# Optimization experiments

Measured on AMD Instinct MI355X. Metric: run time of the kernel, lower is better.

## Reference

```python
import jax, jax.numpy as jnp
import numpy as np

M, N, IN_DIM, NITER = 32, 32, 1024, 100
ALPHA, SIGMA = 0.3, 16.0  # sigma default = max(m, n) / 2
BATCH = 16384


def setup_inputs() -> dict:
    key = jax.random.key(0)
    k1, k2 = jax.random.split(key)
    x = jax.random.normal(k1, (BATCH, IN_DIM), dtype=jnp.float32)
    weights = jax.random.normal(k2, (IN_DIM, M * N), dtype=jnp.float32)
    ii, jj = jnp.meshgrid(jnp.arange(M), jnp.arange(N), indexing='ij')
    locations = jnp.stack([ii.ravel(), jj.ravel()], axis=1).astype(jnp.int32)  # (m*n, 2), row-major like the generator
    return {"x": x, "weights": weights, "locations": locations, "current_iter": 10}


def reference(x, weights, locations, current_iter):
    # x: (B, in_dim); weights: (in_dim, m*n); locations: (m*n, 2)
    B = x.shape[0]
    # Euclidean distances from each sample to each neuron, via ||a-b||^2 expansion
    x2 = jnp.sum(x * x, axis=1, keepdims=True)            # (B, 1)
    w2 = jnp.sum(weights * weights, axis=0)[None, :]      # (1, m*n)
    d2 = jnp.clip(x2 + w2 - 2.0 * (x @ weights), 0.0, None)
    dists = jnp.sqrt(d2)                                  # (B, m*n)
    loss_per = jnp.min(dists, axis=1)                     # (B,)
    bmu_index = jnp.argmin(dists, axis=1)                 # (B,)
    iter_correction = 1.0 - current_iter / NITER
    lr = ALPHA * iter_correction
    sigma = SIGMA * iter_correction
    loc_f = locations.astype(jnp.float32)                 # (m*n, 2)
    bmu_loc = loc_f[bmu_index]                            # (B, 2)
    # squared grid distance of every neuron to each sample's BMU
    dsq = jnp.sum((loc_f[None, :, :] - bmu_loc[:, None, :]) ** 2, axis=2)  # (B, m*n)
    lr_locations = jnp.exp(-dsq / (sigma * sigma)) * lr   # (B, m*n)
    # delta[i,k] = (1/B) * sum_b lr_locations[b,k] * (x[b,i] - weights[i,k])
    # computed without materializing the (B, in_dim, m*n) broadcast tensor
    pos = jnp.einsum('bk,bi->ik', lr_locations, x)        # (in_dim, m*n)
    neg = weights * jnp.sum(lr_locations, axis=0)[None, :]
    delta = (pos - neg) / B
    new_weights = weights + delta
    loss = jnp.sum(loss_per) / B
    return loss, new_weights
```

## Files before the change

### kernel.cpp

```cpp
#include <hip/hip_runtime.h>

typedef unsigned short u16;
typedef short bf16x8 __attribute__((ext_vector_type(8)));
typedef float f32x4 __attribute__((ext_vector_type(4)));

#define BATCH   16384
#define INDIM   1024
#define KNEUR   1024

__device__ __forceinline__ u16 f2bf(float f) {
  union { float f; unsigned u; } v; v.f = f;
  unsigned r = v.u + 0x7FFFu + ((v.u >> 16) & 1u);
  return (u16)(r >> 16);
}
__device__ __forceinline__ float bf2f(u16 h) {
  union { unsigned u; float f; } v; v.u = ((unsigned)h) << 16; return v.f;
}

#define GLDS(gp, lp) __builtin_amdgcn_global_load_lds( \
  (const __attribute__((address_space(1))) void*)(gp), \
  (__attribute__((address_space(3))) void*)(lp), 16, 0, 0)

__global__ void k_conv_x(const float* __restrict__ x, u16* __restrict__ xb,
                         float* __restrict__ x2) {
  int b = blockIdx.x;
  int t = threadIdx.x;
  const float4 v = *(const float4*)(x + (size_t)b * INDIM + t * 4);
  u16 o0 = f2bf(v.x), o1 = f2bf(v.y), o2 = f2bf(v.z), o3 = f2bf(v.w);
  ushort4 o; o.x = o0; o.y = o1; o.z = o2; o.w = o3;
  *(ushort4*)(xb + (size_t)b * INDIM + t * 4) = o;
  float s = v.x * v.x + v.y * v.y + v.z * v.z + v.w * v.w;
  for (int m = 32; m; m >>= 1) s += __shfl_xor(s, m, 64);
  __shared__ float ws_[4];
  if ((t & 63) == 0) ws_[t >> 6] = s;
  __syncthreads();
  if (t == 0) x2[b] = ws_[0] + ws_[1] + ws_[2] + ws_[3];
}

__global__ void k_trans_w(const float* __restrict__ w, u16* __restrict__ wt) {
  __shared__ float tile[64][65];
  int bi = blockIdx.x & 15;
  int bj = blockIdx.x >> 4;
  int tx = threadIdx.x & 63, ty = threadIdx.x >> 6;
  int i0 = bj * 64, k0 = bi * 64;
  for (int r = ty; r < 64; r += 4)
    tile[r][tx] = w[(size_t)(i0 + r) * KNEUR + k0 + tx];
  __syncthreads();
  for (int r = ty; r < 64; r += 4)
    wt[(size_t)(k0 + r) * INDIM + i0 + tx] = f2bf(tile[tx][r]);
}

__global__ void k_w2(const float* __restrict__ w, float* __restrict__ w2) {
  int tx = threadIdx.x & 63, ty = threadIdx.x >> 6;
  int k = blockIdx.x * 64 + tx;
  float s = 0.f;
  for (int i = ty * 256; i < ty * 256 + 256; ++i) {
    float v = w[(size_t)i * KNEUR + k];
    s += v * v;
  }
  __shared__ float red[4][64];
  red[ty][tx] = s;
  __syncthreads();
  if (ty == 0) w2[k] = red[0][tx] + red[1][tx] + red[2][tx] + red[3][tx];
}

__global__ void k_T(const int* __restrict__ loc, const int* __restrict__ itp,
                    u16* __restrict__ Tb, float* __restrict__ Tf) {
  int id = blockIdx.x * 256 + threadIdx.x;
  int c = id >> 10, k = id & 1023;
  float corr = 1.f - (float)itp[0] / 100.f;
  float lr = 0.3f * corr;
  float sig = 16.f * corr;
  float inv_s2 = 1.f / (sig * sig);
  int di = loc[2 * c] - loc[2 * k];
  int dj = loc[2 * c + 1] - loc[2 * k + 1];
  float v = lr * __expf(-(float)(di * di + dj * dj) * inv_s2);
  Tf[id] = v;
  Tb[id] = f2bf(v);
}

template <int EPI>
__global__ __launch_bounds__(256, 2)
void k_gemm(const u16* __restrict__ A, const u16* __restrict__ Bm,
            const float* __restrict__ x2, const float* __restrict__ w2,
            float* __restrict__ pmin, int* __restrict__ pidx,
            const float* __restrict__ Wf, const float* __restrict__ S,
            float* __restrict__ outw) {
  __shared__ __align__(16) u16 ldsA[128 * 64];
  __shared__ __align__(16) u16 ldsB[128 * 64];
  __shared__ float s_rv[2][128];
  __shared__ int   s_ri[2][128];

  int bid = blockIdx.x;
  int mb, nb;
  if (EPI == 1) {
    int swz = (bid & 7) * 128 + (bid >> 3);
    mb = swz >> 3; nb = swz & 7;
  } else {
    mb = bid >> 3; nb = bid & 7;
  }
  int lane = threadIdx.x & 63;
  int wid = threadIdx.x >> 6;
  int wr = wid >> 1, wc = wid & 1;

  f32x4 acc[4][4];
  #pragma unroll
  for (int i = 0; i < 4; ++i)
    #pragma unroll
    for (int j = 0; j < 4; ++j) { acc[i][j][0] = 0.f; acc[i][j][1] = 0.f; acc[i][j][2] = 0.f; acc[i][j][3] = 0.f; }

  const size_t rowA0 = (size_t)mb * 128;
  const size_t rowB0 = (size_t)nb * 128;

  for (int kt = 0; kt < 16; ++kt) {
    int k0 = kt * 64;
    __syncthreads();
    #pragma unroll
    for (int q = 0; q < 4; ++q) {
      int p = q * 256 + wid * 64 + lane;
      int row = p >> 3;
      int clog = (p & 7) ^ (row & 7);
      GLDS(A + (rowA0 + row) * 1024 + k0 + clog * 8,
           ldsA + (size_t)(q * 256 + wid * 64) * 8);
    }
    #pragma unroll
    for (int q = 0; q < 4; ++q) {
      int p = q * 256 + wid * 64 + lane;
      int row = p >> 3;
      int clog = (p & 7) ^ (row & 7);
      GLDS(Bm + (rowB0 + row) * 1024 + k0 + clog * 8,
           ldsB + (size_t)(q * 256 + wid * 64) * 8);
    }
    __syncthreads();
    #pragma unroll
    for (int kk = 0; kk < 2; ++kk) {
      bf16x8 af[4], bfr[4];
      #pragma unroll
      for (int mt = 0; mt < 4; ++mt) {
        int row = wr * 64 + mt * 16 + (lane & 15);
        int ch = (kk * 4 + (lane >> 4)) ^ (row & 7);
        af[mt] = *(const bf16x8*)(ldsA + row * 64 + ch * 8);
      }
      #pragma unroll
      for (int nt = 0; nt < 4; ++nt) {
        int row = wc * 64 + nt * 16 + (lane & 15);
        int ch = (kk * 4 + (lane >> 4)) ^ (row & 7);
        bfr[nt] = *(const bf16x8*)(ldsB + row * 64 + ch * 8);
      }
      #pragma unroll
      for (int mt = 0; mt < 4; ++mt)
        #pragma unroll
        for (int nt = 0; nt < 4; ++nt)
          acc[mt][nt] = __builtin_amdgcn_mfma_f32_16x16x32_bf16(af[mt], bfr[nt], acc[mt][nt], 0, 0, 0);
    }
  }

  if (EPI == 1) {
    int g = lane >> 4;
    int li = lane & 15;
    #pragma unroll
    for (int mt = 0; mt < 4; ++mt) {
      #pragma unroll
      for (int r = 0; r < 4; ++r) {
        int rowl = wr * 64 + mt * 16 + g * 4 + r;
        float xv = x2[rowA0 + rowl];
        float v = 1e30f; int vi = 0;
        #pragma unroll
        for (int nt = 0; nt < 4; ++nt) {
          int col = (int)rowB0 + wc * 64 + nt * 16 + li;
          float d2 = xv + w2[col] - 2.f * acc[mt][nt][r];
          if (d2 < v) { v = d2; vi = col; }
        }
        #pragma unroll
        for (int m = 1; m < 16; m <<= 1) {
          float ov = __shfl_xor(v, m, 64);
          int oi = __shfl_xor(vi, m, 64);
          if (ov < v || (ov == v && oi < vi)) { v = ov; vi = oi; }
        }
        if (li == 0) { s_rv[wc][rowl] = v; s_ri[wc][rowl] = vi; }
      }
    }
    __syncthreads();
    int t = threadIdx.x;
    if (t < 128) {
      float v0 = s_rv[0][t], v1 = s_rv[1][t];
      int i0 = s_ri[0][t], i1 = s_ri[1][t];
      float v = v0; int vi = i0;
      if (v1 < v0) { v = v1; vi = i1; }
      size_t brow = rowA0 + t;
      pmin[brow * 8 + nb] = v;
      pidx[brow * 8 + nb] = vi;
    }
  } else {
    const float invB = 1.f / (float)BATCH;
    #pragma unroll
    for (int mt = 0; mt < 4; ++mt)
      #pragma unroll
      for (int nt = 0; nt < 4; ++nt)
        #pragma unroll
        for (int r = 0; r < 4; ++r) {
          int i = (int)rowA0 + wr * 64 + mt * 16 + (lane >> 4) * 4 + r;
          int k = (int)rowB0 + wc * 64 + nt * 16 + (lane & 15);
          float wv = Wf[(size_t)i * KNEUR + k];
          float P = acc[mt][nt][r];
          outw[(size_t)i * KNEUR + k] = wv + (P - wv * S[k]) * invB;
        }
  }
}

__global__ void k_bmu(const float* __restrict__ pmin, const int* __restrict__ pidx,
                      int* __restrict__ bmu, float* __restrict__ lpart) {
  int b = blockIdx.x * 256 + threadIdx.x;
  float v = 1e30f; int vi = 0;
  #pragma unroll
  for (int j = 0; j < 8; ++j) {
    float pv = pmin[(size_t)b * 8 + j];
    if (pv < v) { v = pv; vi = pidx[(size_t)b * 8 + j]; }
  }
  bmu[b] = vi;
  float d = sqrtf(fmaxf(v, 0.f));
  __shared__ float red[256];
  red[threadIdx.x] = d;
  __syncthreads();
  for (int s = 128; s > 0; s >>= 1) {
    if (threadIdx.x < s) red[threadIdx.x] += red[threadIdx.x + s];
    __syncthreads();
  }
  if (threadIdx.x == 0) lpart[blockIdx.x] = red[0];
}

__global__ void k_loss(const float* __restrict__ lpart, float* __restrict__ out) {
  if (threadIdx.x == 0) {
    float s = 0.f;
    for (int i = 0; i < 64; ++i) s += lpart[i];
    out[0] = s * (1.f / (float)BATCH);
  }
}

__global__ __launch_bounds__(256)
void k_xsum(const int* __restrict__ bmu, const u16* __restrict__ xb,
            u16* __restrict__ xst, float* __restrict__ cntf) {
  int c = blockIdx.x;
  int t = threadIdx.x;
  __shared__ u16 list[BATCH];
  __shared__ int scan[256];
  __shared__ int s_total;
  int cnt = 0;
  for (int j = 0; j < 64; ++j) cnt += (bmu[j * 256 + t] == c);
  scan[t] = cnt;
  __syncthreads();
  for (int off = 1; off < 256; off <<= 1) {
    int v = scan[t];
    int va = (t >= off) ? scan[t - off] : 0;
    __syncthreads();
    scan[t] = v + va;
    __syncthreads();
  }
  int pos = scan[t] - cnt;
  if (t == 255) s_total = scan[255];
  __syncthreads();
  int total = s_total;
  for (int j = 0; j < 64; ++j) {
    int b = j * 256 + t;
    if (bmu[b] == c) list[pos++] = (u16)b;
  }
  __syncthreads();
  float a0 = 0.f, a1 = 0.f, a2 = 0.f, a3 = 0.f;
  for (int m = 0; m < total; ++m) {
    int b = list[m];
    ushort4 v = *(const ushort4*)(xb + (size_t)b * INDIM + t * 4);
    a0 += bf2f(v.x); a1 += bf2f(v.y); a2 += bf2f(v.z); a3 += bf2f(v.w);
  }
  xst[(size_t)(4 * t + 0) * KNEUR + c] = f2bf(a0);
  xst[(size_t)(4 * t + 1) * KNEUR + c] = f2bf(a1);
  xst[(size_t)(4 * t + 2) * KNEUR + c] = f2bf(a2);
  xst[(size_t)(4 * t + 3) * KNEUR + c] = f2bf(a3);
  if (t == 0) cntf[c] = (float)total;
}

__global__ void k_spart(const float* __restrict__ cntf, const float* __restrict__ Tf,
                        float* __restrict__ spart) {
  int cchunk = blockIdx.x >> 2;
  int kb = blockIdx.x & 3;
  int k = kb * 256 + threadIdx.x;
  float s = 0.f;
  for (int c = cchunk * 64; c < cchunk * 64 + 64; ++c)
    s += cntf[c] * Tf[(size_t)c * KNEUR + k];
  spart[cchunk * KNEUR + k] = s;
}
__global__ void k_sfinal(const float* __restrict__ spart, float* __restrict__ S) {
  int k = blockIdx.x * 256 + threadIdx.x;
  float s = 0.f;
  #pragma unroll
  for (int j = 0; j < 16; ++j) s += spart[j * KNEUR + k];
  S[k] = s;
}

extern "C" void kernel_launch(void* const* d_in, const int* in_sizes, int n_in,
                              void* d_out, int out_size, void* d_ws, size_t ws_size,
                              hipStream_t stream) {
  const float* x = (const float*)d_in[0];
  const float* w = (const float*)d_in[1];
  const int* loc = (const int*)d_in[2];
  const int* it = (const int*)d_in[3];
  float* out = (float*)d_out;

  char* ws = (char*)d_ws;
  size_t off = 0;
  auto alloc = [&](size_t bytes) -> void* {
    void* p = ws + off;
    off += (bytes + 255) & ~(size_t)255;
    return p;
  };
  u16* xb    = (u16*)  alloc((size_t)BATCH * INDIM * 2);
  u16* wt    = (u16*)  alloc((size_t)KNEUR * INDIM * 2);
  u16* Tb    = (u16*)  alloc((size_t)KNEUR * KNEUR * 2);
  float* Tf  = (float*)alloc((size_t)KNEUR * KNEUR * 4);
  u16* xst   = (u16*)  alloc((size_t)INDIM * KNEUR * 2);
  float* x2  = (float*)alloc((size_t)BATCH * 4);
  float* w2  = (float*)alloc((size_t)KNEUR * 4);
  float* pmin= (float*)alloc((size_t)BATCH * 8 * 4);
  int* pidx  = (int*)  alloc((size_t)BATCH * 8 * 4);
  int* bmu   = (int*)  alloc((size_t)BATCH * 4);
  float* cntf= (float*)alloc((size_t)KNEUR * 4);
  float* spart=(float*)alloc((size_t)16 * KNEUR * 4);
  float* S   = (float*)alloc((size_t)KNEUR * 4);
  float* lpart=(float*)alloc(64 * 4);
  if (off > ws_size) return;

  k_conv_x<<<BATCH, 256, 0, stream>>>(x, xb, x2);
  k_trans_w<<<256, 256, 0, stream>>>(w, wt);
  k_w2<<<16, 256, 0, stream>>>(w, w2);
  k_T<<<4096, 256, 0, stream>>>(loc, it, Tb, Tf);
  k_gemm<1><<<1024, 256, 0, stream>>>(xb, wt, x2, w2, pmin, pidx, nullptr, nullptr, nullptr);
  k_bmu<<<64, 256, 0, stream>>>(pmin, pidx, bmu, lpart);
  k_loss<<<1, 64, 0, stream>>>(lpart, out);
  k_xsum<<<1024, 256, 0, stream>>>(bmu, xb, xst, cntf);
  k_spart<<<64, 256, 0, stream>>>(cntf, Tf, spart);
  k_sfinal<<<4, 256, 0, stream>>>(spart, S);
  k_gemm<0><<<64, 256, 0, stream>>>(xst, Tb, nullptr, nullptr, nullptr, nullptr, w, S, out + 1);
}
```

Baseline: 165.2 us.

## Replace per-neuron BMU scan with counting-sort permutation and atomic segmented sums

The per-BMU x-sum is restructured. Before, each of 1024 blocks scanned all 16384 BMU indices to build its own member list. Now a global histogram, a prefix scan and an atomic placement build a permutation sorted by BMU. Blocks then sum contiguous 16-sample chunks and flush partial sums to an fp32 buffer with atomics, and a tiled transpose produces the bf16 xst layout. This removes the redundant full scan done in every block and the load imbalance across neurons, at the cost of extra launches, a 4MB zeroing pass, fp32 atomics and a non-deterministic summation order.

```diff
diff --git a/kernel.cpp b/kernel.cpp
--- a/kernel.cpp
+++ b/kernel.cpp
@@ -237,45 +237,82 @@
   }
 }
 
+__global__ void k_zero(float* __restrict__ p, int n) {
+  int i = blockIdx.x * 256 + threadIdx.x;
+  if (i < n) p[i] = 0.f;
+}
+
+__global__ void k_count(const int* __restrict__ bmu, int* __restrict__ cnt) {
+  int b = blockIdx.x * 256 + threadIdx.x;
+  atomicAdd(&cnt[bmu[b]], 1);
+}
+
+__global__ void k_offsets(const int* __restrict__ cnt, int* __restrict__ cursor,
+                          float* __restrict__ cntf) {
+  __shared__ int s[1024];
+  int t = threadIdx.x;
+  int v = cnt[t];
+  cntf[t] = (float)v;
+  s[t] = v;
+  __syncthreads();
+  for (int off = 1; off < 1024; off <<= 1) {
+    int a = s[t];
+    int b = (t >= off) ? s[t - off] : 0;
+    __syncthreads();
+    s[t] = a + b;
+    __syncthreads();
+  }
+  cursor[t] = s[t] - v;
+}
+
+__global__ void k_place(const int* __restrict__ bmu, int* __restrict__ cursor,
+                        int* __restrict__ perm) {
+  int b = blockIdx.x * 256 + threadIdx.x;
+  int c = bmu[b];
+  int p = atomicAdd(&cursor[c], 1);
+  perm[p] = b;
+}
+
 __global__ __launch_bounds__(256)
-void k_xsum(const int* __restrict__ bmu, const u16* __restrict__ xb,
-            u16* __restrict__ xst, float* __restrict__ cntf) {
-  int c = blockIdx.x;
+void k_xsum2(const int* __restrict__ perm, const int* __restrict__ bmu,
+             const u16* __restrict__ xb, float* __restrict__ Xf) {
   int t = threadIdx.x;
-  __shared__ u16 list[BATCH];
-  __shared__ int scan[256];
-  __shared__ int s_total;
-  int cnt = 0;
-  for (int j = 0; j < 64; ++j) cnt += (bmu[j * 256 + t] == c);
-  scan[t] = cnt;
-  __syncthreads();
-  for (int off = 1; off < 256; off <<= 1) {
-    int v = scan[t];
-    int va = (t >= off) ? scan[t - off] : 0;
-    __syncthreads();
-    scan[t] = v + va;
-    __syncthreads();
-  }
-  int pos = scan[t] - cnt;
-  if (t == 255) s_total = scan[255];
-  __syncthreads();
-  int total = s_total;
-  for (int j = 0; j < 64; ++j) {
-    int b = j * 256 + t;
-    if (bmu[b] == c) list[pos++] = (u16)b;
-  }
-  __syncthreads();
+  int m0 = blockIdx.x * 16;
+  int pm[16], cl[16];
+  #pragma unroll
+  for (int j = 0; j < 16; ++j) pm[j] = perm[m0 + j];
+  #pragma unroll
+  for (int j = 0; j < 16; ++j) cl[j] = bmu[pm[j]];
   float a0 = 0.f, a1 = 0.f, a2 = 0.f, a3 = 0.f;
-  for (int m = 0; m < total; ++m) {
-    int b = list[m];
-    ushort4 v = *(const ushort4*)(xb + (size_t)b * INDIM + t * 4);
+  int ccur = cl[0];
+  #pragma unroll
+  for (int j = 0; j < 16; ++j) {
+    if (cl[j] != ccur) {
+      float* p = Xf + (size_t)ccur * INDIM + 4 * t;
+      atomicAdd(p + 0, a0); atomicAdd(p + 1, a1);
+      atomicAdd(p + 2, a2); atomicAdd(p + 3, a3);
+      a0 = a1 = a2 = a3 = 0.f;
+      ccur = cl[j];
+    }
+    ushort4 v = *(const ushort4*)(xb + (size_t)pm[j] * INDIM + t * 4);
     a0 += bf2f(v.x); a1 += bf2f(v.y); a2 += bf2f(v.z); a3 += bf2f(v.w);
   }
-  xst[(size_t)(4 * t + 0) * KNEUR + c] = f2bf(a0);
-  xst[(size_t)(4 * t + 1) * KNEUR + c] = f2bf(a1);
-  xst[(size_t)(4 * t + 2) * KNEUR + c] = f2bf(a2);
-  xst[(size_t)(4 * t + 3) * KNEUR + c] = f2bf(a3);
-  if (t == 0) cntf[c] = (float)total;
+  float* p = Xf + (size_t)ccur * INDIM + 4 * t;
+  atomicAdd(p + 0, a0); atomicAdd(p + 1, a1);
+  atomicAdd(p + 2, a2); atomicAdd(p + 3, a3);
+}
+
+__global__ void k_xst_trans(const float* __restrict__ Xf, u16* __restrict__ xst) {
+  __shared__ float tile[64][65];
+  int bc = blockIdx.x & 15;
+  int bi = blockIdx.x >> 4;
+  int tx = threadIdx.x & 63, ty = threadIdx.x >> 6;
+  int c0 = bc * 64, i0 = bi * 64;
+  for (int r = ty; r < 64; r += 4)
+    tile[r][tx] = Xf[(size_t)(c0 + r) * INDIM + i0 + tx];
+  __syncthreads();
+  for (int r = ty; r < 64; r += 4)
+    xst[(size_t)(i0 + r) * KNEUR + c0 + tx] = f2bf(tile[tx][r]);
 }
 
 __global__ void k_spart(const float* __restrict__ cntf, const float* __restrict__ Tf,
@@ -326,16 +363,26 @@
   float* spart=(float*)alloc((size_t)16 * KNEUR * 4);
   float* S   = (float*)alloc((size_t)KNEUR * 4);
   float* lpart=(float*)alloc(64 * 4);
+  float* Xf  = (float*)alloc((size_t)KNEUR * INDIM * 4);
+  int* cnt   = (int*)  alloc((size_t)KNEUR * 4);
+  int* cursor= (int*)  alloc((size_t)KNEUR * 4);
+  int* perm  = (int*)  alloc((size_t)BATCH * 4);
   if (off > ws_size) return;
 
   k_conv_x<<<BATCH, 256, 0, stream>>>(x, xb, x2);
   k_trans_w<<<256, 256, 0, stream>>>(w, wt);
   k_w2<<<16, 256, 0, stream>>>(w, w2);
   k_T<<<4096, 256, 0, stream>>>(loc, it, Tb, Tf);
+  k_zero<<<(KNEUR * INDIM + 255) / 256, 256, 0, stream>>>(Xf, KNEUR * INDIM);
+  k_zero<<<8, 256, 0, stream>>>((float*)cnt, 2 * KNEUR);
   k_gemm<1><<<1024, 256, 0, stream>>>(xb, wt, x2, w2, pmin, pidx, nullptr, nullptr, nullptr);
   k_bmu<<<64, 256, 0, stream>>>(pmin, pidx, bmu, lpart);
   k_loss<<<1, 64, 0, stream>>>(lpart, out);
-  k_xsum<<<1024, 256, 0, stream>>>(bmu, xb, xst, cntf);
+  k_count<<<64, 256, 0, stream>>>(bmu, cnt);
+  k_offsets<<<1, 1024, 0, stream>>>(cnt, cursor, cntf);
+  k_place<<<64, 256, 0, stream>>>(bmu, cursor, perm);
+  k_xsum2<<<BATCH / 16, 256, 0, stream>>>(perm, bmu, xb, Xf);
+  k_xst_trans<<<256, 256, 0, stream>>>(Xf, xst);
   k_spart<<<64, 256, 0, stream>>>(cntf, Tf, spart);
   k_sfinal<<<4, 256, 0, stream>>>(spart, S);
   k_gemm<0><<<64, 256, 0, stream>>>(xst, Tb, nullptr, nullptr, nullptr, nullptr, w, S, out + 1);
```

Measured after the change: 171.9 us. 4.1% more time.
